# Kernel optimization log

Hardware: AMD Instinct MI355X
Metric: run time of the kernel (lower is better)

The kernel has to match this reference:

```python
import jax, jax.numpy as jnp
import numpy as np

LN_EPS = 1e-5
DELTA_FACTOR = 0.01
PATCH_KH, PATCH_KW = 4, 4
SIGMA = 2.0


def layernorm(x, g, b):
    m = jnp.mean(x, axis=-1, keepdims=True)
    v = jnp.var(x, axis=-1, keepdims=True)
    return (x - m) * jax.lax.rsqrt(v + LN_EPS) * g + b


def grid_sample(src, grid):
    # src [B,C,H,W], grid [B,Hg,Wg,2] in [-1,1]; bilinear, align_corners=False, zero padding
    B, C, H, W = src.shape
    Hg, Wg = grid.shape[1], grid.shape[2]
    gx = (grid[..., 0] + 1.0) * (W * 0.5) - 0.5
    gy = (grid[..., 1] + 1.0) * (H * 0.5) - 0.5
    x0 = jnp.floor(gx)
    y0 = jnp.floor(gy)
    wx = gx - x0
    wy = gy - y0
    x0i = x0.astype(jnp.int32)
    y0i = y0.astype(jnp.int32)
    flat = src.reshape(B, C, H * W)

    def tap(xi, yi, w):
        valid = (xi >= 0) & (xi < W) & (yi >= 0) & (yi < H)
        idx = (jnp.clip(yi, 0, H - 1) * W + jnp.clip(xi, 0, W - 1)).reshape(B, -1)
        vals = jax.vmap(lambda f, i: f[:, i])(flat, idx)  # [B,C,Hg*Wg]
        return vals * (w * valid).reshape(B, 1, -1)

    out = (tap(x0i, y0i, (1 - wx) * (1 - wy)) + tap(x0i + 1, y0i, wx * (1 - wy))
           + tap(x0i, y0i + 1, (1 - wx) * wy) + tap(x0i + 1, y0i + 1, wx * wy))
    return out.reshape(B, C, Hg, Wg)


def gaussian_filt(x, k, sigma):
    # depthwise Gaussian blur, NCHW
    C = x.shape[1]
    coords = jnp.arange(k, dtype=x.dtype) - (k - 1) / 2.0
    g2 = jnp.exp(-(coords[:, None] ** 2 + coords[None, :] ** 2) / (2.0 * sigma ** 2))
    g2 = g2 / g2.sum()
    kern = jnp.broadcast_to(g2, (C, 1, k, k))
    p = (k - 1) // 2
    return jax.lax.conv_general_dilated(x, kern, (1, 1), [(p, p), (p, p)],
                                        dimension_numbers=('NCHW', 'OIHW', 'NCHW'),
                                        feature_group_count=C)


def reconstruct_feature(feature, mask, k, sigma):
    if k <= 1:
        return feature
    feature = feature * mask
    out = gaussian_filt(jnp.concatenate([feature, mask], axis=1), k, sigma)
    f_i = out[:, :-1]
    m_i = out[:, -1:]
    f_i = f_i / (m_i + 1e-6)
    f_i = f_i * (m_i > 0)
    return feature + (1 - mask) * f_i


def token2map(x, loc, H, W, k, sigma):
    B, N, C = x.shape
    l = jnp.clip(loc, 0.0, 1.0) * jnp.array([W - 1, H - 1], dtype=loc.dtype)
    l = jnp.round(l).astype(jnp.int32)
    idx = l[..., 0] + l[..., 1] * W + (jnp.arange(B, dtype=jnp.int32) * (H * W))[:, None]
    vals = jnp.concatenate([x, jnp.ones((B, N, 1), x.dtype)], axis=-1).reshape(B * N, C + 1)
    out = jnp.zeros((B * H * W, C + 1), x.dtype).at[idx.reshape(-1)].add(vals)
    out = out.reshape(B, H, W, C + 1).transpose(0, 3, 1, 2)
    feat, mask = out[:, :-1], out[:, -1:]
    feat = feat / (mask + 1e-6)
    mask = (mask > 0).astype(x.dtype)
    feat = feat * mask
    return reconstruct_feature(feat, mask, k, sigma)


def forward(x, loc, src, H, W, kernel_size,
            w_delta, b_delta, norm1_g, norm1_b, conv_w, conv_b,
            norm2_g, norm2_b, fc1_w, fc1_b, fc2_w, fc2_b):
    B, N, _ = loc.shape
    Cs, Hs, Ws = src.shape[1], src.shape[2], src.shape[3]
    delta = (layernorm(x, norm1_g, norm1_b) @ w_delta + b_delta) * DELTA_FACTOR
    loc_extra = jnp.clip(loc + delta, 0.0, 1.0)
    # extract_local_feature: 4x4 sub-pixel patch around each extra location
    xo = (jnp.arange(PATCH_KW, dtype=loc.dtype) - (PATCH_KW - 1) / 2.0) / (Ws - 1)
    yo = (jnp.arange(PATCH_KH, dtype=loc.dtype) - (PATCH_KH - 1) / 2.0) / (Hs - 1)
    off = jnp.stack([jnp.broadcast_to(xo[None, :], (PATCH_KH, PATCH_KW)),
                     jnp.broadcast_to(yo[:, None], (PATCH_KH, PATCH_KW))], axis=-1)
    grid = (loc_extra[:, :, None, None, :] + off[None, None]) * 2.0 - 1.0  # [B,N,kh,kw,2]
    patches = grid_sample(src, grid.reshape(B, N, PATCH_KH * PATCH_KW, 2))  # [B,C,N,kh*kw]
    patches = patches.reshape(B, Cs, N, PATCH_KH, PATCH_KW)
    # local_conv: 4x4 conv stride 4 over a 4x4 patch == single dot product
    extra = jnp.einsum('bcnhw,ochw->bno', patches, conv_w) + conv_b
    extra = layernorm(extra, norm2_g, norm2_b)
    # token2map scatter + gaussian reconstruction, then gather back at loc_extra
    fmap = token2map(x, loc, H, W, kernel_size, SIGMA)
    extra_inter = grid_sample(fmap, (loc_extra * 2.0 - 1.0)[:, None, :, :])  # [B,C,1,N]
    extra_inter = extra_inter[:, :, 0].transpose(0, 2, 1)  # [B,N,C]
    extra = jnp.concatenate([extra_inter, extra], axis=-1)
    h = jax.nn.gelu(extra @ fc1_w + fc1_b, approximate=False)
    extra = h @ fc2_w + fc2_b
    return jnp.concatenate([x, extra], axis=1), jnp.concatenate([loc, loc_extra], axis=1)


def setup_inputs() -> dict:
    key = jax.random.key(0)
    ks = jax.random.split(key, 12)
    B, N, D = 4, 16384, 256
    LD, HID = 64, 4 * D
    inp = {
        'x': jax.random.normal(ks[0], (B, N, D), jnp.float32),
        'loc': jax.random.uniform(ks[1], (B, N, 2), jnp.float32),
        'src': jax.random.normal(ks[2], (B, 3, 512, 512), jnp.float32),
        'pos_embed': jnp.zeros((1,), jnp.float32),
        'H': 128, 'W': 128, 'kernel_size': 3,
        'w_delta': jax.random.normal(ks[3], (D, 2), jnp.float32) * 0.02,
        'b_delta': jnp.zeros((2,), jnp.float32),
        'norm1_g': jnp.ones((D,), jnp.float32),
        'norm1_b': jnp.zeros((D,), jnp.float32),
        'conv_w': jax.random.normal(ks[4], (LD, 3, 4, 4), jnp.float32) * 0.1,
        'conv_b': jnp.zeros((LD,), jnp.float32),
        'norm2_g': jnp.ones((LD,), jnp.float32),
        'norm2_b': jnp.zeros((LD,), jnp.float32),
        'fc1_w': jax.random.normal(ks[5], (D + LD, HID), jnp.float32) * 0.02,
        'fc1_b': jnp.zeros((HID,), jnp.float32),
        'fc2_w': jax.random.normal(ks[6], (HID, D), jnp.float32) * 0.02,
        'fc2_b': jnp.zeros((D,), jnp.float32),
    }
    return inp


def reference(x, loc, src, pos_embed, H, W, kernel_size,
              w_delta, b_delta, norm1_g, norm1_b, conv_w, conv_b,
              norm2_g, norm2_b, fc1_w, fc1_b, fc2_w, fc2_b):
    # pos_embed is accepted by the torch forward but never used
    return forward(x, loc, src, H, W, kernel_size,
                   w_delta, b_delta, norm1_g, norm1_b, conv_w, conv_b,
                   norm2_g, norm2_b, fc1_w, fc1_b, fc2_w, fc2_b)
```

## Files before the change

kernel.cpp:

```cpp
#include <hip/hip_runtime.h>
#include <hip/hip_bf16.h>

#define B_    4
#define N_    16384
#define D_    256
#define LD_   64
#define HID_  1024
#define HW_   128
#define HSRC_ 512
#define CS_   3
#define KIN_  320

typedef __attribute__((ext_vector_type(8))) short bf16x8;
typedef __attribute__((ext_vector_type(4))) float f32x4;

__device__ __forceinline__ float wsum(float v) {
#pragma unroll
  for (int off = 32; off; off >>= 1) v += __shfl_xor(v, off, 64);
  return v;
}

__device__ __forceinline__ unsigned short f2bf(float f) {
  unsigned int u = __float_as_uint(f);
  u = (u + 0x7fffu + ((u >> 16) & 1u)) >> 16;
  return (unsigned short)u;
}
__device__ __forceinline__ float b2f(unsigned short u) {
  return __uint_as_float(((unsigned int)u) << 16);
}

__device__ __forceinline__ float gelu_f(float x) {
  float z = 0.7978845608028654f * (x + 0.044715f * x * x * x);
  float e = __expf(2.0f * z);
  float th = 1.0f - 2.0f / (e + 1.0f);
  return 0.5f * x * (1.0f + th);
}

__device__ __forceinline__ void async16(unsigned short* lds, const unsigned short* g) {
  __builtin_amdgcn_global_load_lds(
      (const __attribute__((address_space(1))) unsigned int*)g,
      (__attribute__((address_space(3))) unsigned int*)lds, 16, 0, 0);
}

__global__ __launch_bounds__(256) void k_wconv(const float* __restrict__ fc1w,
                                               const float* __restrict__ fc2w,
                                               unsigned short* __restrict__ bt1,
                                               unsigned short* __restrict__ bt2) {
  int i = blockIdx.x * 256 + threadIdx.x;
  if (i < KIN_ * HID_) {
    int n = i / KIN_, k = i % KIN_;
    bt1[i] = f2bf(fc1w[(size_t)k * HID_ + n]);
  } else {
    int j = i - KIN_ * HID_;
    if (j < D_ * HID_) {
      int n = j / HID_, k = j % HID_;
      bt2[j] = f2bf(fc2w[(size_t)k * D_ + n]);
    }
  }
}

__global__ __launch_bounds__(256) void k_delta(const float* __restrict__ x,
                                               const float* __restrict__ loc,
                                               const float* __restrict__ wd,
                                               const float* __restrict__ bd,
                                               const float* __restrict__ g1,
                                               const float* __restrict__ b1,
                                               float* __restrict__ locex,
                                               float* __restrict__ out1,
                                               float* __restrict__ out0,
                                               int* __restrict__ head,
                                               int* __restrict__ nxt) {
  int wv = threadIdx.x >> 6, lane = threadIdx.x & 63;
  int t = blockIdx.x * 4 + wv;
  int b = t >> 14, n = t & (N_ - 1);
  const float4 xv = *(const float4*)(x + (size_t)t * D_ + lane * 4);
  *(float4*)(out0 + ((size_t)b * 2 * N_ + n) * D_ + lane * 4) = xv;
  float m = wsum(xv.x + xv.y + xv.z + xv.w) * (1.0f / D_);
  float d0 = xv.x - m, d1 = xv.y - m, d2 = xv.z - m, d3 = xv.w - m;
  float v = wsum(d0 * d0 + d1 * d1 + d2 * d2 + d3 * d3) * (1.0f / D_);
  float r = rsqrtf(v + 1e-5f);
  const float4 gv = *(const float4*)(g1 + lane * 4);
  const float4 bv = *(const float4*)(b1 + lane * 4);
  float n0 = d0 * r * gv.x + bv.x;
  float n1 = d1 * r * gv.y + bv.y;
  float n2 = d2 * r * gv.z + bv.z;
  float n3 = d3 * r * gv.w + bv.w;
  int i2 = lane * 8;
  float p0 = n0 * wd[i2 + 0] + n1 * wd[i2 + 2] + n2 * wd[i2 + 4] + n3 * wd[i2 + 6];
  float p1 = n0 * wd[i2 + 1] + n1 * wd[i2 + 3] + n2 * wd[i2 + 5] + n3 * wd[i2 + 7];
  p0 = wsum(p0);
  p1 = wsum(p1);
  if (lane == 0) {
    float lx = loc[(size_t)t * 2], ly = loc[(size_t)t * 2 + 1];
    float ex = fminf(fmaxf(lx + (p0 + bd[0]) * 0.01f, 0.0f), 1.0f);
    float ey = fminf(fmaxf(ly + (p1 + bd[1]) * 0.01f, 0.0f), 1.0f);
    locex[(size_t)t * 2] = ex;
    locex[(size_t)t * 2 + 1] = ey;
    size_t o1 = (size_t)b * 2 * N_;
    out1[(o1 + n) * 2 + 0] = lx;
    out1[(o1 + n) * 2 + 1] = ly;
    out1[(o1 + N_ + n) * 2 + 0] = ex;
    out1[(o1 + N_ + n) * 2 + 1] = ey;
    float cx = fminf(fmaxf(lx, 0.0f), 1.0f) * 127.0f;
    float cy = fminf(fmaxf(ly, 0.0f), 1.0f) * 127.0f;
    int ix = (int)rintf(cx);
    int iy = (int)rintf(cy);
    int cell = (b << 14) + iy * HW_ + ix;
    nxt[t] = atomicExch(head + cell, t);
  }
}

__global__ __launch_bounds__(256) void k_gather(const float* __restrict__ x,
                                                const int* __restrict__ head,
                                                const int* __restrict__ nxt,
                                                unsigned short* __restrict__ featn,
                                                float* __restrict__ cntf) {
  int cell = blockIdx.x;
  int tid = threadIdx.x;
  __shared__ int toks[16];
  __shared__ int scount, snext;
  float acc = 0.0f;
  int total = 0;
  int cur = head[cell];
  while (cur >= 0) {
    if (tid == 0) {
      int c = 0, p = cur;
      while (p >= 0 && c < 16) {
        toks[c++] = p;
        p = nxt[p];
      }
      scount = c;
      snext = p;
    }
    __syncthreads();
    int c = scount;
    for (int i = 0; i < c; ++i) acc += x[(size_t)toks[i] * D_ + tid];
    total += c;
    cur = snext;
    __syncthreads();
  }
  featn[(size_t)cell * D_ + tid] = f2bf((total > 0) ? acc / ((float)total + 1e-6f) : 0.0f);
  if (tid == 0) cntf[cell] = (float)total;
}

__global__ __launch_bounds__(256) void k_filter(const unsigned short* __restrict__ featn,
                                                const float* __restrict__ cntf,
                                                unsigned short* __restrict__ fmap) {
  int pix = blockIdx.x;
  int c = threadIdx.x;
  int b = pix >> 14;
  int p = pix & 16383;
  int y = p >> 7, xc = p & 127;
  float cc = cntf[pix];
  unsigned short outv;
  if (cc > 0.0f) {
    outv = featn[(size_t)pix * D_ + c];
  } else {
    float e1 = expf(-0.125f), e2 = expf(-0.25f);
    float sumw = 1.0f + 4.0f * e1 + 4.0f * e2;
    float gf = 0.0f, gm = 0.0f;
#pragma unroll
    for (int dy = -1; dy <= 1; ++dy)
#pragma unroll
      for (int dx = -1; dx <= 1; ++dx) {
        int ny = y + dy, nx = xc + dx;
        if (ny < 0 || ny >= HW_ || nx < 0 || nx >= HW_) continue;
        int q = (b << 14) + ny * HW_ + nx;
        if (cntf[q] > 0.0f) {
          int dd = dy * dy + dx * dx;
          float w = (dd == 0 ? 1.0f : (dd == 1 ? e1 : e2)) / sumw;
          gf += w * b2f(featn[(size_t)q * D_ + c]);
          gm += w;
        }
      }
    outv = f2bf((gm > 0.0f) ? gf / (gm + 1e-6f) : 0.0f);
  }
  fmap[(size_t)pix * D_ + c] = outv;
}

__global__ __launch_bounds__(256) void k_patch(const float* __restrict__ src,
                                               const float* __restrict__ locex,
                                               const float* __restrict__ convw,
                                               const float* __restrict__ convb,
                                               const float* __restrict__ g2,
                                               const float* __restrict__ b2,
                                               unsigned short* __restrict__ ecat) {
  __shared__ float cw[LD_ * 49];
  __shared__ float patch[4][48];
  for (int i = threadIdx.x; i < LD_ * 48; i += 256)
    cw[(i / 48) * 49 + (i % 48)] = convw[i];
  int wv = threadIdx.x >> 6, lane = threadIdx.x & 63;
  int t = blockIdx.x * 4 + wv;
  int b = t >> 14;
  float ex = locex[(size_t)t * 2], ey = locex[(size_t)t * 2 + 1];
  __syncthreads();
  if (lane < 48) {
    int c = lane >> 4, p = lane & 15, py = p >> 2, px = p & 3;
    float u = ex + ((float)px - 1.5f) / 511.0f;
    float vv = ey + ((float)py - 1.5f) / 511.0f;
    float gx = u * 512.0f - 0.5f;
    float gy = vv * 512.0f - 0.5f;
    float fx = floorf(gx), fy = floorf(gy);
    float wx = gx - fx, wy = gy - fy;
    int x0 = (int)fx, y0 = (int)fy;
    const float* plane = src + (size_t)(b * CS_ + c) * (HSRC_ * HSRC_);
    float acc = 0.0f;
#pragma unroll
    for (int ty = 0; ty < 2; ++ty)
#pragma unroll
      for (int tx = 0; tx < 2; ++tx) {
        int xi = x0 + tx, yi = y0 + ty;
        float w = (tx ? wx : 1.0f - wx) * (ty ? wy : 1.0f - wy);
        if (xi >= 0 && xi < HSRC_ && yi >= 0 && yi < HSRC_)
          acc += w * plane[yi * HSRC_ + xi];
      }
    patch[wv][lane] = acc;
  }
  __syncthreads();
  float e = convb[lane];
#pragma unroll
  for (int i = 0; i < 48; ++i) e += patch[wv][i] * cw[lane * 49 + i];
  float m = wsum(e) * (1.0f / 64.0f);
  float d = e - m;
  float v = wsum(d * d) * (1.0f / 64.0f);
  float val = d * rsqrtf(v + 1e-5f) * g2[lane] + b2[lane];
  ecat[(size_t)t * KIN_ + D_ + lane] = f2bf(val);
}

__global__ __launch_bounds__(256) void k_sample(const unsigned short* __restrict__ fmap,
                                                const float* __restrict__ locex,
                                                unsigned short* __restrict__ ecat) {
  int wv = threadIdx.x >> 6, lane = threadIdx.x & 63;
  int t = blockIdx.x * 4 + wv;
  int b = t >> 14;
  float gx = locex[(size_t)t * 2] * 128.0f - 0.5f;
  float gy = locex[(size_t)t * 2 + 1] * 128.0f - 0.5f;
  float fx = floorf(gx), fy = floorf(gy);
  float wx = gx - fx, wy = gy - fy;
  int x0 = (int)fx, y0 = (int)fy;
  const unsigned short* base = fmap + (((size_t)b << 14)) * D_;
  float4 acc = {0.0f, 0.0f, 0.0f, 0.0f};
#pragma unroll
  for (int ty = 0; ty < 2; ++ty)
#pragma unroll
    for (int tx = 0; tx < 2; ++tx) {
      int xi = x0 + tx, yi = y0 + ty;
      float w = (tx ? wx : 1.0f - wx) * (ty ? wy : 1.0f - wy);
      if (xi >= 0 && xi < HW_ && yi >= 0 && yi < HW_) {
        ushort4 f = *(const ushort4*)(base + (size_t)(yi * HW_ + xi) * D_ + lane * 4);
        acc.x += w * b2f(f.x);
        acc.y += w * b2f(f.y);
        acc.z += w * b2f(f.z);
        acc.w += w * b2f(f.w);
      }
    }
  ushort4 o;
  o.x = f2bf(acc.x);
  o.y = f2bf(acc.y);
  o.z = f2bf(acc.z);
  o.w = f2bf(acc.w);
  *(ushort4*)(ecat + (size_t)t * KIN_ + lane * 4) = o;
}

template <int GELU>
__global__ __launch_bounds__(256) void k_gemm128(const unsigned short* __restrict__ A,
                                                 const unsigned short* __restrict__ Bt,
                                                 const float* __restrict__ bias, int K,
                                                 int Nn, unsigned short* __restrict__ hout,
                                                 float* __restrict__ out0) {
  __shared__ __align__(16) unsigned short sh[16384];
  unsigned short* As = sh;
  unsigned short* Bs = sh + 8192;
  int tid = threadIdx.x, wv = tid >> 6, lane = tid & 63;
  int wm = wv & 1, wn = wv >> 1;

  int nt_cnt = gridDim.x;
  int lin = blockIdx.y * nt_cnt + blockIdx.x;
  int xcd = lin & 7;
  int slot = lin >> 3;
  int tile_n = (slot % nt_cnt) * 128;
  int tile_m = ((slot / nt_cnt) * 8 + xcd) * 128;

  f32x4 acc[4][4];
#pragma unroll
  for (int i = 0; i < 4; ++i)
#pragma unroll
    for (int j = 0; j < 4; ++j) acc[i][j] = (f32x4){0.0f, 0.0f, 0.0f, 0.0f};

  int srow = tid >> 3;
  int schunk = (tid & 7) ^ (srow & 7);
  const unsigned short* ga = A + (size_t)(tile_m + srow) * K + schunk * 8;
  const unsigned short* gb = Bt + (size_t)(tile_n + srow) * K + schunk * 8;
  size_t skip = (size_t)32 * K;
  int lofs = tid * 8;

  int ar = wm * 64 + (lane & 15);
  int br = wn * 64 + (lane & 15);
  int ksel = lane >> 4;
  int sw = lane & 7;

  for (int k0 = 0; k0 < K; k0 += 64) {
#pragma unroll
    for (int c = 0; c < 4; ++c) async16(As + c * 2048 + lofs, ga + c * skip);
#pragma unroll
    for (int c = 0; c < 4; ++c) async16(Bs + c * 2048 + lofs, gb + c * skip);
    ga += 64;
    gb += 64;
    __syncthreads();
#pragma unroll
    for (int j = 0; j < 2; ++j) {
      bf16x8 afr[4], bfr[4];
      int ca = ((j * 4 + ksel) ^ sw) * 8;
#pragma unroll
      for (int i = 0; i < 4; ++i) {
        afr[i] = *(const bf16x8*)(As + (ar + i * 16) * 64 + ca);
        bfr[i] = *(const bf16x8*)(Bs + (br + i * 16) * 64 + ca);
      }
#pragma unroll
      for (int mt = 0; mt < 4; ++mt)
#pragma unroll
        for (int nt = 0; nt < 4; ++nt)
          acc[mt][nt] =
              __builtin_amdgcn_mfma_f32_16x16x32_bf16(afr[mt], bfr[nt], acc[mt][nt], 0, 0, 0);
    }
    __syncthreads();
  }

  if (GELU) {
#pragma unroll
    for (int nt = 0; nt < 4; ++nt) {
      int nl = wn * 64 + nt * 16 + (lane & 15);
      float bv = bias[tile_n + nl];
#pragma unroll
      for (int mt = 0; mt < 4; ++mt) {
        int ml = wm * 64 + mt * 16 + (lane >> 4) * 4;
#pragma unroll
        for (int r = 0; r < 4; ++r)
          sh[(ml + r) * 128 + nl] = f2bf(gelu_f(acc[mt][nt][r] + bv));
      }
    }
    __syncthreads();
#pragma unroll
    for (int it = 0; it < 8; ++it) {
      int idx = it * 256 + tid;
      int row = idx >> 4, ch = (idx & 15) * 8;
      *(uint4*)(hout + (size_t)(tile_m + row) * Nn + tile_n + ch) =
          *(const uint4*)(sh + row * 128 + ch);
    }
  } else {
#pragma unroll
    for (int nt = 0; nt < 4; ++nt) {
      int n = tile_n + wn * 64 + nt * 16 + (lane & 15);
      float bv = bias[n];
#pragma unroll
      for (int mt = 0; mt < 4; ++mt) {
        int mbase = tile_m + wm * 64 + mt * 16 + (lane >> 4) * 4;
#pragma unroll
        for (int r = 0; r < 4; ++r) {
          int m = mbase + r;
          float v = acc[mt][nt][r] + bv;
          int bb = m >> 14, ntok = m & (N_ - 1);
          out0[((size_t)bb * 2 * N_ + N_ + ntok) * D_ + n] = v;
        }
      }
    }
  }
}

extern "C" void kernel_launch(void* const* d_in, const int* in_sizes, int n_in,
                              void* d_out, int out_size, void* d_ws, size_t ws_size,
                              hipStream_t stream) {
  const float* x = (const float*)d_in[0];
  const float* loc = (const float*)d_in[1];
  const float* src = (const float*)d_in[2];
  const float* wd = (const float*)d_in[7];
  const float* bd = (const float*)d_in[8];
  const float* g1 = (const float*)d_in[9];
  const float* b1 = (const float*)d_in[10];
  const float* cw = (const float*)d_in[11];
  const float* cb = (const float*)d_in[12];
  const float* g2 = (const float*)d_in[13];
  const float* b2 = (const float*)d_in[14];
  const float* fc1w = (const float*)d_in[15];
  const float* fc1b = (const float*)d_in[16];
  const float* fc2w = (const float*)d_in[17];
  const float* fc2b = (const float*)d_in[18];

  float* out0 = (float*)d_out;
  float* out1 = out0 + (size_t)B_ * 2 * N_ * D_;

  char* ws = (char*)d_ws;
  unsigned short* featn = (unsigned short*)(ws + 0);
  unsigned short* fmap = (unsigned short*)(ws + 33554432);
  unsigned short* h = (unsigned short*)(ws + 0);
  unsigned short* ecat = (unsigned short*)(ws + 134217728);
  unsigned short* bt1 = (unsigned short*)(ws + 176160768);
  unsigned short* bt2 = (unsigned short*)(ws + 176816128);
  float* cntf = (float*)(ws + 177340416);
  float* locex = (float*)(ws + 177602560);
  int* head = (int*)(ws + 178126848);
  int* nxt = (int*)(ws + 178388992);

  hipMemsetAsync(head, 0xFF, (size_t)262144, stream);

  k_wconv<<<2304, 256, 0, stream>>>(fc1w, fc2w, bt1, bt2);
  k_delta<<<16384, 256, 0, stream>>>(x, loc, wd, bd, g1, b1, locex, out1, out0, head, nxt);
  k_gather<<<65536, 256, 0, stream>>>(x, head, nxt, featn, cntf);
  k_filter<<<65536, 256, 0, stream>>>(featn, cntf, fmap);
  k_patch<<<16384, 256, 0, stream>>>(src, locex, cw, cb, g2, b2, ecat);
  k_sample<<<16384, 256, 0, stream>>>(fmap, locex, ecat);
  k_gemm128<1><<<dim3(8, 512), 256, 0, stream>>>(ecat, bt1, fc1b, KIN_, HID_, h, nullptr);
  k_gemm128<0><<<dim3(2, 512), 256, 0, stream>>>(h, bt2, fc2b, HID_, D_, nullptr, out0);
}
```

Baseline: 565.0 us.

## Double-buffer LDS tiles in GEMM to overlap async loads with MFMA

```diff
diff --git a/kernel.cpp b/kernel.cpp
--- a/kernel.cpp
+++ b/kernel.cpp
@@ -268,9 +268,7 @@
                                                  const float* __restrict__ bias, int K,
                                                  int Nn, unsigned short* __restrict__ hout,
                                                  float* __restrict__ out0) {
-  __shared__ __align__(16) unsigned short sh[16384];
-  unsigned short* As = sh;
-  unsigned short* Bs = sh + 8192;
+  __shared__ __align__(16) unsigned short sh[32768];
   int tid = threadIdx.x, wv = tid >> 6, lane = tid & 63;
   int wm = wv & 1, wn = wv >> 1;
 
@@ -299,14 +297,35 @@
   int ksel = lane >> 4;
   int sw = lane & 7;
 
-  for (int k0 = 0; k0 < K; k0 += 64) {
-#pragma unroll
-    for (int c = 0; c < 4; ++c) async16(As + c * 2048 + lofs, ga + c * skip);
-#pragma unroll
-    for (int c = 0; c < 4; ++c) async16(Bs + c * 2048 + lofs, gb + c * skip);
-    ga += 64;
-    gb += 64;
-    __syncthreads();
+  int nk = K >> 6;
+
+#pragma unroll
+  for (int c = 0; c < 4; ++c) async16(sh + c * 2048 + lofs, ga + c * skip);
+#pragma unroll
+  for (int c = 0; c < 4; ++c) async16(sh + 8192 + c * 2048 + lofs, gb + c * skip);
+  ga += 64;
+  gb += 64;
+
+  int cur = 0;
+  for (int k0 = 0; k0 < nk; ++k0) {
+    __builtin_amdgcn_sched_barrier(0);
+    if (k0 + 1 < nk) {
+      unsigned short* nb = sh + (cur ^ 16384);
+#pragma unroll
+      for (int c = 0; c < 4; ++c) async16(nb + c * 2048 + lofs, ga + c * skip);
+#pragma unroll
+      for (int c = 0; c < 4; ++c) async16(nb + 8192 + c * 2048 + lofs, gb + c * skip);
+      ga += 64;
+      gb += 64;
+      asm volatile("s_waitcnt vmcnt(8)" ::: "memory");
+    } else {
+      asm volatile("s_waitcnt vmcnt(0)" ::: "memory");
+    }
+    __builtin_amdgcn_s_barrier();
+    __builtin_amdgcn_sched_barrier(0);
+
+    const unsigned short* As = sh + cur;
+    const unsigned short* Bs = As + 8192;
 #pragma unroll
     for (int j = 0; j < 2; ++j) {
       bf16x8 afr[4], bfr[4];
@@ -323,8 +342,11 @@
           acc[mt][nt] =
               __builtin_amdgcn_mfma_f32_16x16x32_bf16(afr[mt], bfr[nt], acc[mt][nt], 0, 0, 0);
     }
-    __syncthreads();
-  }
+    __builtin_amdgcn_sched_barrier(0);
+    __builtin_amdgcn_s_barrier();
+    cur ^= 16384;
+  }
+  __builtin_amdgcn_sched_barrier(0);
 
   if (GELU) {
 #pragma unroll
```

Result: faster. 544.0 us (-3.7%).
